# Optimization experiments

Hardware: AMD Instinct MI355X
Metric: run time of the kernel (lower is better)

The kernel has to match this reference:

```python
import jax, jax.numpy as jnp
import numpy as np

B, S, D = 4, 2048, 1024
NEG_INF = jnp.float32(-jnp.inf)


def setup_inputs() -> dict:
    key = jax.random.key(0)
    kx, kq, kk, kv = jax.random.split(key, 4)
    scale = 0.02
    return {
        "x": jax.random.normal(kx, (B, S, D), dtype=jnp.float32),
        "Wq": jax.random.normal(kq, (D, D), dtype=jnp.float32) * scale,
        "Wk": jax.random.normal(kk, (D, D), dtype=jnp.float32) * scale,
        "Wv": jax.random.normal(kv, (D, D), dtype=jnp.float32) * scale,
    }


def reference(x, Wq, Wk, Wv):
    # nn.Linear(d_in, d_out): y = x @ W.T (no bias; qkv_bias=False)
    q = jnp.einsum("bsd,ed->bse", x, Wq)
    k = jnp.einsum("bsd,ed->bse", x, Wk)
    v = jnp.einsum("bsd,ed->bse", x, Wv)
    n = x.shape[1]
    scores = jnp.einsum("bqe,bke->bqk", q, k)  # [B, S, S]
    # causal mask: positions k > q are masked with -inf
    causal = jnp.tril(jnp.ones((n, n), dtype=bool))
    scores = jnp.where(causal[None, :, :], scores, NEG_INF)
    attn = jax.nn.softmax(scores / jnp.sqrt(jnp.float32(k.shape[-1])), axis=-1)
    # dropout p=0.0 (eval) -> identity
    return jnp.einsum("bqk,bke->bqe", attn, v)
```

## Files before the change

kernel.cpp:

```cpp
#include <hip/hip_runtime.h>
#include <hip/hip_bf16.h>
#include <stdint.h>
#include <stddef.h>


typedef __hip_bfloat16 bf16;
typedef short short8 __attribute__((ext_vector_type(8)));
typedef short short4v __attribute__((ext_vector_type(4)));
typedef float f32x4 __attribute__((ext_vector_type(4)));

#define BM 128
#define BN 128
#define BK 64
#define MSZ 8192
#define DD 1024

__device__ __forceinline__ void cstore(float* p, float v) { *p = v; }
__device__ __forceinline__ void cstore(bf16* p, float v) { *p = __float2bfloat16(v); }

__global__ __launch_bounds__(256)
void f2b(const float* __restrict__ s, bf16* __restrict__ d, int n) {
  const int i = (blockIdx.x * 256 + threadIdx.x) * 4;
  if (i >= n) return;
  const float4 v = *(const float4*)(s + i);
  bf16 t[4] = {__float2bfloat16(v.x), __float2bfloat16(v.y),
               __float2bfloat16(v.z), __float2bfloat16(v.w)};
  *(short4v*)(d + i) = *(short4v*)t;
}

__global__ __launch_bounds__(256)
void f2b3(const float* __restrict__ a, const float* __restrict__ b,
          const float* __restrict__ c, bf16* __restrict__ d, int n) {
  const float* s = (blockIdx.y == 0) ? a : (blockIdx.y == 1) ? b : c;
  const int i = (blockIdx.x * 256 + threadIdx.x) * 4;
  if (i >= n) return;
  const float4 v = *(const float4*)(s + i);
  bf16 t[4] = {__float2bfloat16(v.x), __float2bfloat16(v.y),
               __float2bfloat16(v.z), __float2bfloat16(v.w)};
  *(short4v*)(d + (size_t)blockIdx.y * n + i) = *(short4v*)t;
}

template <int MODE, typename CT>
__global__ __launch_bounds__(256, 3)
void gemm_bt(const bf16* __restrict__ A, const bf16* __restrict__ B,
             CT* __restrict__ C, bf16* __restrict__ C2,
             int lda, int ldb, int ldc, int K,
             long sA, long sB, long sC, float scale) {
  int by, bx;
  if (MODE == 2) {
    const int t = blockIdx.x;
    by = (int)((__fsqrt_rn(8.f * (float)t + 1.f) - 1.f) * 0.5f);
    while ((by + 1) * (by + 2) / 2 <= t) by++;
    while (by * (by + 1) / 2 > t) by--;
    bx = t - by * (by + 1) / 2;
  } else if (MODE == 3) {
    by = gridDim.y - 1 - blockIdx.y;
    bx = blockIdx.x;
  } else {
    by = blockIdx.y;
    bx = blockIdx.x;
  }

  __shared__ short8 As[8 * 128];
  __shared__ short8 Bs[8 * 128];

  const int tid = threadIdx.x;
  const int wave = tid >> 6, lane = tid & 63;
  const int wm = wave >> 1, wn = wave & 1;
  const int l15 = lane & 15, q4 = lane >> 4;
  const int bm0 = by * BM, bn0 = bx * BN;

  const bf16* Az = A + (long)blockIdx.z * sA;
  const bf16* Bz = B + (long)blockIdx.z * sB;
  CT* Cz = C + (long)blockIdx.z * sC;

  const int kg = (lane >> 3) & 7;
  const int rl = wave * 8 + (lane & 7);

  const bf16* apg = Az + (size_t)(bm0 + rl) * lda + kg * 8;
  const bf16* bpg = Bz + (size_t)(bn0 + rl) * ldb + kg * 8;
  const size_t la32 = (size_t)32 * lda, lb32 = (size_t)32 * ldb;
  short8* dstA = &As[kg * 128 + rl];
  short8* dstB = &Bs[kg * 128 + rl];

  const int Ke = (MODE == 3) ? min(K, (by + 1) * BM) : K;

  f32x4 acc[4][4] = {};
  short8 ra[4], rb[4];

#pragma unroll
  for (int j = 0; j < 4; j++) {
    ra[j] = *(const short8*)(apg + j * la32);
    rb[j] = *(const short8*)(bpg + j * lb32);
  }

  for (int k0 = 0; k0 < Ke; k0 += BK) {
    __syncthreads();
#pragma unroll
    for (int j = 0; j < 4; j++) {
      dstA[j * 32] = ra[j];
      dstB[j * 32] = rb[j];
    }
    __syncthreads();

    const int kn = k0 + BK;
    if (kn < Ke) {
#pragma unroll
      for (int j = 0; j < 4; j++) {
        ra[j] = *(const short8*)(apg + j * la32 + kn);
        rb[j] = *(const short8*)(bpg + j * lb32 + kn);
      }
    }

#pragma unroll
    for (int s = 0; s < 2; s++) {
      const int ch = (s * 4 + q4) * 128;
      short8 af[4], bfr[4];
#pragma unroll
      for (int i = 0; i < 4; i++)
        af[i] = As[ch + wm * 64 + i * 16 + l15];
#pragma unroll
      for (int j = 0; j < 4; j++)
        bfr[j] = Bs[ch + wn * 64 + j * 16 + l15];
#pragma unroll
      for (int i = 0; i < 4; i++)
#pragma unroll
        for (int j = 0; j < 4; j++)
          acc[i][j] = __builtin_amdgcn_mfma_f32_16x16x32_bf16(af[i], bfr[j], acc[i][j], 0, 0, 0);
    }
  }

  if (MODE == 1 && bx >= 16) {
#pragma unroll
    for (int i = 0; i < 4; i++) {
#pragma unroll
      for (int j = 0; j < 4; j++) {
        const int rowb = bm0 + wm * 64 + i * 16 + q4 * 4;
        const int v = (bn0 - 2048) + wn * 64 + j * 16 + l15;
        bf16 t[4] = {__float2bfloat16(acc[i][j][0]), __float2bfloat16(acc[i][j][1]),
                     __float2bfloat16(acc[i][j][2]), __float2bfloat16(acc[i][j][3])};
        *(short4v*)(C2 + (size_t)v * MSZ + rowb) = *(short4v*)t;
      }
    }
    return;
  }

  CT* Cb = Cz;
  int coff = bn0;
  if (MODE == 1) {
    Cb = Cz + (bx >= 8 ? (size_t)MSZ * DD : 0);
    coff = (bx & 7) * BN;
  }
#pragma unroll
  for (int i = 0; i < 4; i++) {
#pragma unroll
    for (int j = 0; j < 4; j++) {
#pragma unroll
      for (int r = 0; r < 4; r++) {
        const int row = bm0 + wm * 64 + i * 16 + q4 * 4 + r;
        const int col = coff + wn * 64 + j * 16 + l15;
        cstore(&Cb[(size_t)row * ldc + col], acc[i][j][r] * scale);
      }
    }
  }
}

__global__ __launch_bounds__(256)
void softmax_rows(const bf16* __restrict__ Sc, bf16* __restrict__ P, int S) {
  const int q = blockIdx.x, b = blockIdx.y;
  const short8* srow = (const short8*)(Sc + ((size_t)b * S + q) * S);
  short8* prow = (short8*)(P + ((size_t)b * S + q) * S);
  const int len = q + 1;
  const int tid = threadIdx.x;
  const int wave = tid >> 6, lane = tid & 63;
  __shared__ float red[10];

  const short8 raw = srow[tid];
  float v[8];
#pragma unroll
  for (int j = 0; j < 8; j++) {
    const int k = tid * 8 + j;
    const float f = __bfloat162float(((const bf16*)&raw)[j]);
    v[j] = (k < len) ? f : -1e30f;
  }

  float m = v[0];
#pragma unroll
  for (int j = 1; j < 8; j++) m = fmaxf(m, v[j]);
#pragma unroll
  for (int o = 32; o; o >>= 1) m = fmaxf(m, __shfl_down(m, o));
  if (lane == 0) red[wave] = m;
  __syncthreads();
  if (tid == 0) red[8] = fmaxf(fmaxf(red[0], red[1]), fmaxf(red[2], red[3]));
  __syncthreads();
  const float M = red[8];

  float e[8], s = 0.f;
#pragma unroll
  for (int j = 0; j < 8; j++) { e[j] = __expf(v[j] - M); s += e[j]; }
#pragma unroll
  for (int o = 32; o; o >>= 1) s += __shfl_down(s, o);
  if (lane == 0) red[4 + wave] = s;
  __syncthreads();
  if (tid == 0) red[9] = red[4] + red[5] + red[6] + red[7];
  __syncthreads();
  const float inv = 1.f / red[9];

  short8 outp;
#pragma unroll
  for (int j = 0; j < 8; j++) {
    const int k = tid * 8 + j;
    ((bf16*)&outp)[j] = __float2bfloat16((k < len) ? e[j] * inv : 0.f);
  }
  prow[tid] = outp;
}

extern "C" void kernel_launch(void* const* d_in, const int* in_sizes, int n_in,
                              void* d_out, int out_size, void* d_ws, size_t ws_size,
                              hipStream_t stream) {
  const float* x  = (const float*)d_in[0];
  const float* Wq = (const float*)d_in[1];
  const float* Wk = (const float*)d_in[2];
  const float* Wv = (const float*)d_in[3];
  float* out = (float*)d_out;

  const int Bb = 4, S = 2048, D = 1024, MS = Bb * S;

  char* ws = (char*)d_ws;
  bf16* xb = (bf16*)ws;
  bf16* wb = (bf16*)(ws + (size_t)MS * D * 2);
  bf16* Q  = (bf16*)(ws + (size_t)MS * D * 2 + 3u * D * D * 2);
  bf16* Kp = Q + (size_t)MS * D;
  bf16* VT = Kp + (size_t)MS * D;
  bf16* Sc = VT + (size_t)MS * D;
  bf16* P  = (bf16*)ws;
  (void)Kp;

  dim3 blk(256);

  f2b<<<dim3(MS * D / 4 / 256), blk, 0, stream>>>(x, xb, MS * D);
  f2b3<<<dim3(D * D / 4 / 256, 3), blk, 0, stream>>>(Wq, Wk, Wv, wb, D * D);

  gemm_bt<1, bf16><<<dim3(3 * D / BN, MS / BM, 1), blk, 0, stream>>>(
      xb, wb, Q, VT, D, D, D, D, 0, 0, 0, 1.f);
  gemm_bt<2, bf16><<<dim3(136, 1, Bb), blk, 0, stream>>>(
      Q, Kp, Sc, nullptr, D, D, S, D,
      (long)S * D, (long)S * D, (long)S * S, 0.03125f);
  softmax_rows<<<dim3(S, Bb), blk, 0, stream>>>(Sc, P, S);
  gemm_bt<3, float><<<dim3(D / BN, S / BM, Bb), blk, 0, stream>>>(
      P, VT, out, nullptr, S, MS, D, S,
      (long)S * S, (long)S, (long)S * D, 1.f);
}
```

Measured before the change: 315.5 us.

## Load GEMM tiles directly into LDS via global_load_lds with new smem layout

Replaces the register-staged global-to-LDS copy (prefetch into registers, then store to shared) with direct global_load_lds transfers, and changes the shared-memory tile layout and fragment indexing to match. It also raises the occupancy hint from 3 to 4 blocks per CU, since fewer staging registers are needed. The cost is that the register prefetch overlap is lost: each iteration now waits for the load to land before computing, with a second barrier per k-step.

```diff
diff --git a/kernel.cpp b/kernel.cpp
--- a/kernel.cpp
+++ b/kernel.cpp
@@ -41,7 +41,7 @@
 }
 
 template <int MODE, typename CT>
-__global__ __launch_bounds__(256, 3)
+__global__ __launch_bounds__(256, 4)
 void gemm_bt(const bf16* __restrict__ A, const bf16* __restrict__ B,
              CT* __restrict__ C, bf16* __restrict__ C2,
              int lda, int ldb, int ldc, int K,
@@ -61,8 +61,8 @@
     bx = blockIdx.x;
   }
 
-  __shared__ short8 As[8 * 128];
-  __shared__ short8 Bs[8 * 128];
+  __shared__ short8 As[1024];
+  __shared__ short8 Bs[1024];
 
   const int tid = threadIdx.x;
   const int wave = tid >> 6, lane = tid & 63;
@@ -74,60 +74,44 @@
   const bf16* Bz = B + (long)blockIdx.z * sB;
   CT* Cz = C + (long)blockIdx.z * sC;
 
-  const int kg = (lane >> 3) & 7;
-  const int rl = wave * 8 + (lane & 7);
-
-  const bf16* apg = Az + (size_t)(bm0 + rl) * lda + kg * 8;
-  const bf16* bpg = Bz + (size_t)(bn0 + rl) * ldb + kg * 8;
-  const size_t la32 = (size_t)32 * lda, lb32 = (size_t)32 * ldb;
-  short8* dstA = &As[kg * 128 + rl];
-  short8* dstB = &Bs[kg * 128 + rl];
+  const int sg = lane >> 3, sr = lane & 7;
+  const bf16* apg = Az + (size_t)(bm0 + wave * 32 + sr) * lda + sg * 8;
+  const bf16* bpg = Bz + (size_t)(bn0 + wave * 32 + sr) * ldb + sg * 8;
+  short8* asw = &As[wave * 256];
+  short8* bsw = &Bs[wave * 256];
 
   const int Ke = (MODE == 3) ? min(K, (by + 1) * BM) : K;
 
+  const int rh = l15 >> 3, r3 = l15 & 7;
+  const int fra = wm * 512 + rh * 64 + q4 * 8 + r3;
+  const int frb = wn * 512 + rh * 64 + q4 * 8 + r3;
+
   f32x4 acc[4][4] = {};
-  short8 ra[4], rb[4];
-
-#pragma unroll
-  for (int j = 0; j < 4; j++) {
-    ra[j] = *(const short8*)(apg + j * la32);
-    rb[j] = *(const short8*)(bpg + j * lb32);
-  }
 
   for (int k0 = 0; k0 < Ke; k0 += BK) {
+#pragma unroll
+    for (int j = 0; j < 4; j++) {
+      __builtin_amdgcn_global_load_lds(apg + (size_t)j * 8 * lda + k0,
+                                       asw + j * 64, 16, 0, 0);
+      __builtin_amdgcn_global_load_lds(bpg + (size_t)j * 8 * ldb + k0,
+                                       bsw + j * 64, 16, 0, 0);
+    }
     __syncthreads();
-#pragma unroll
-    for (int j = 0; j < 4; j++) {
-      dstA[j * 32] = ra[j];
-      dstB[j * 32] = rb[j];
-    }
-    __syncthreads();
-
-    const int kn = k0 + BK;
-    if (kn < Ke) {
-#pragma unroll
-      for (int j = 0; j < 4; j++) {
-        ra[j] = *(const short8*)(apg + j * la32 + kn);
-        rb[j] = *(const short8*)(bpg + j * lb32 + kn);
-      }
-    }
 
 #pragma unroll
     for (int s = 0; s < 2; s++) {
-      const int ch = (s * 4 + q4) * 128;
       short8 af[4], bfr[4];
 #pragma unroll
-      for (int i = 0; i < 4; i++)
-        af[i] = As[ch + wm * 64 + i * 16 + l15];
-#pragma unroll
-      for (int j = 0; j < 4; j++)
-        bfr[j] = Bs[ch + wn * 64 + j * 16 + l15];
+      for (int i = 0; i < 4; i++) af[i] = As[fra + i * 128 + s * 32];
+#pragma unroll
+      for (int j = 0; j < 4; j++) bfr[j] = Bs[frb + j * 128 + s * 32];
 #pragma unroll
       for (int i = 0; i < 4; i++)
 #pragma unroll
         for (int j = 0; j < 4; j++)
           acc[i][j] = __builtin_amdgcn_mfma_f32_16x16x32_bf16(af[i], bfr[j], acc[i][j], 0, 0, 0);
     }
+    __syncthreads();
   }
 
   if (MODE == 1 && bx >= 16) {
```

Measured after the change: 314.1 us. Within noise of the previous version (-0.4%).
